# Optimization experiments

Measured on AMD Instinct MI355X. Metric: run time of the kernel, lower is better.

The kernel has to match this reference:

```python
import jax, jax.numpy as jnp
import numpy as np

ALPHA = 0.2
NEG_INF = -9e15


def setup_inputs() -> dict:
    key = jax.random.key(0)
    k1, k2, k3, k4 = jax.random.split(key, 4)
    B, N, C_IN, C_OUT, R, H = 8, 1024, 256, 256, 4, 4
    node_feats = jax.random.normal(k1, (B, N, C_IN), dtype=jnp.float32)
    adj_matrix = jax.random.randint(k2, (B, N, N, R), 0, 2, dtype=jnp.int32)
    # xavier_uniform with gain=1.414 for Linear(c_in, c_out) weights
    lim_w = 1.414 * np.sqrt(6.0 / (C_IN + C_OUT))
    W = jax.random.uniform(k3, (R, C_IN, C_OUT), minval=-lim_w, maxval=lim_w, dtype=jnp.float32)
    c_per = C_OUT // H
    lim_a = 1.414 * np.sqrt(6.0 / (H + 2 * c_per))
    a = jax.random.uniform(k4, (R, H, 2 * c_per), minval=-lim_a, maxval=lim_a, dtype=jnp.float32)
    return {"node_feats": node_feats, "adj_matrix": adj_matrix, "W": W, "a": a}


def reference(node_feats, adj_matrix, W, a):
    B, N, _ = node_feats.shape
    R, H = a.shape[0], a.shape[1]
    C = a.shape[2] // 2  # per-head feature dim
    out = jnp.zeros((B, N, H, C), dtype=node_feats.dtype)
    for r in range(R):
        # per-relation projection: [B,N,H,C]
        f = jnp.einsum('bnc,cd->bnd', node_feats, W[r]).reshape(B, N, H, C)
        a_l, a_r = a[r, :, :C], a[r, :, C:]
        # attention logit decomposes: a . [f_i || f_j] = a_l . f_i + a_r . f_j
        li = jnp.einsum('bnhc,hc->bnh', f, a_l)  # source-node term
        lj = jnp.einsum('bnhc,hc->bnh', f, a_r)  # target-node term
        logits = jax.nn.leaky_relu(li[:, :, None, :] + lj[:, None, :, :], ALPHA)  # [B,N,N,H]
        mask = adj_matrix[..., r] != 0  # [B,N,N]
        logits = jnp.where(mask[..., None], logits, NEG_INF)
        probs = jax.nn.softmax(logits, axis=2)
        out = out + jnp.einsum('bijh,bjhc->bihc', probs, f)
    # concat_heads=True
    return out.reshape(B, N, H * C)
```

## Files before the change

kernel.cpp:

```cpp
#include <hip/hip_runtime.h>
#include <math.h>

#define Bsz 8
#define Nn 1024
#define CIN 256
#define COUT 256
#define NR 4
#define NH 4

typedef unsigned short u16;
typedef __attribute__((ext_vector_type(8))) short bf16x8;
typedef __attribute__((ext_vector_type(4))) float f32x4;
typedef __attribute__((ext_vector_type(2))) float f32x2;

#define OFF_LIP (16u << 20)
#define OFF_LJP ((16u << 20) + (512u << 10))
#define OFF_ADJM (17u << 20)
#define OFF_XBF (21u << 20)
#define OFF_WBFT (25u << 20)
#define OFF_WAL ((25u << 20) + (512u << 10))
#define OFF_WAR ((25u << 20) + (528u << 10))

#define LOG2E 1.4426950408889634f

__device__ __forceinline__ short f2bf(float x) {
  union { float f; unsigned u; } v; v.f = x;
  unsigned r = (v.u + 0x7FFFu + ((v.u >> 16) & 1u)) >> 16;
  return (short)r;
}

__device__ __forceinline__ float fast_exp2(float x) {
#if __has_builtin(__builtin_amdgcn_exp2f)
  return __builtin_amdgcn_exp2f(x);
#else
  return exp2f(x);
#endif
}

__device__ __forceinline__ int sbfe1(unsigned v, int bit) {
#if __has_builtin(__builtin_amdgcn_sbfe)
  return __builtin_amdgcn_sbfe((int)v, bit, 1);
#else
  return ((int)(v << (31 - bit))) >> 31;
#endif
}

__device__ __forceinline__ unsigned perm_hi16(unsigned hi, unsigned lo) {
#if __has_builtin(__builtin_amdgcn_perm)
  return __builtin_amdgcn_perm(hi, lo, 0x07060302u);
#else
  return (lo >> 16) | (hi & 0xFFFF0000u);
#endif
}

__device__ __forceinline__ void gl_lds16(const void* g, void* l) {
  __builtin_amdgcn_global_load_lds(
      (const __attribute__((address_space(1))) unsigned int*)(unsigned long long)g,
      (__attribute__((address_space(3))) unsigned int*)(unsigned int)(unsigned long long)l,
      16, 0, 0);
}

__global__ __launch_bounds__(256, 8)
void gatt_pack(const int4* __restrict__ adj4, unsigned long long* __restrict__ adjm) {
  const int t = threadIdx.x;
  const int wid = blockIdx.x * 4 + (t >> 6);
  const int lane = t & 63;
  const int jw = wid & 15;
  const int i = (wid >> 4) & 1023;
  const int b = wid >> 14;
  const int j = jw * 64 + lane;
  const int4 av = adj4[(size_t)(b * Nn + i) * Nn + j];
  const unsigned long long b0 = __ballot(av.x != 0);
  const unsigned long long b1 = __ballot(av.y != 0);
  const unsigned long long b2 = __ballot(av.z != 0);
  const unsigned long long b3 = __ballot(av.w != 0);
  if (lane < 4) {
    unsigned long long v = (lane == 0) ? b0 : (lane == 1) ? b1 : (lane == 2) ? b2 : b3;
    adjm[((size_t)((b * Nn + i) * NR + lane)) * 16 + jw] = v;
  }
}

__global__ __launch_bounds__(256, 4)
void gatt_prep(const float* __restrict__ W, const float* __restrict__ a,
               u16* __restrict__ WbfT, float* __restrict__ wa_l,
               float* __restrict__ wa_r) {
  const int t = threadIdx.x;
  if (blockIdx.x < 32) {
    const int r = blockIdx.x >> 3, kc = blockIdx.x & 7;
    u16 pk[32];
#pragma unroll 8
    for (int kk = 0; kk < 32; ++kk)
      pk[kk] = (u16)f2bf(W[(size_t)r * 65536 + (size_t)(kc * 32 + kk) * COUT + t]);
    u16* dst = WbfT + (size_t)r * 65536 + (size_t)t * CIN + kc * 32;
#pragma unroll
    for (int q = 0; q < 4; ++q) *(int4*)(dst + q * 8) = *(int4*)(pk + q * 8);
  } else {
    const int cb = blockIdx.x - 32;
    const int r = cb >> 2, h = cb & 3;
    float sl = 0.f, sr = 0.f;
    const float* Wp = W + (size_t)r * 65536 + (size_t)t * COUT + h * 64;
    const float* ap = a + r * 512 + h * 128;
#pragma unroll 8
    for (int c = 0; c < 64; ++c) {
      const float wv = Wp[c];
      sl = fmaf(wv, ap[c], sl);
      sr = fmaf(wv, ap[64 + c], sr);
    }
    wa_l[(size_t)cb * CIN + t] = sl;
    wa_r[(size_t)cb * CIN + t] = sr;
  }
}

__global__ __launch_bounds__(256, 4)
void gatt_logitx(const float* __restrict__ X, const float4* __restrict__ wal4,
                 const float4* __restrict__ war4, float* __restrict__ Lip,
                 float* __restrict__ Ljp, u16* __restrict__ Xbf) {
  __shared__ float Xs[16 * 260];
  const int t = threadIdx.x;
  const int row0 = blockIdx.x * 16;
  {
    const int il = t >> 4, kq = t & 15;
    const float4* xp = (const float4*)(X + (size_t)(row0 + il) * CIN + kq * 16);
    float4 v[4];
    u16 pk[16];
#pragma unroll
    for (int u = 0; u < 4; ++u) {
      v[u] = xp[u];
      pk[u * 4 + 0] = (u16)f2bf(v[u].x);
      pk[u * 4 + 1] = (u16)f2bf(v[u].y);
      pk[u * 4 + 2] = (u16)f2bf(v[u].z);
      pk[u * 4 + 3] = (u16)f2bf(v[u].w);
    }
    float4* dst = (float4*)(Xs + il * 260 + kq * 16);
#pragma unroll
    for (int u = 0; u < 4; ++u) dst[u] = v[u];
    u16* xb = Xbf + (size_t)(row0 + il) * CIN + kq * 16;
    *(int4*)xb = *(int4*)pk;
    *(int4*)(xb + 8) = *(int4*)(pk + 8);
  }
  __syncthreads();
  const int rl = t >> 4, combo = t & 15;
  float li = 0.f, lj = 0.f;
#pragma unroll 8
  for (int k4 = 0; k4 < 64; ++k4) {
    const float4 x4 = *(const float4*)(Xs + rl * 260 + k4 * 4);
    const float4 wl = wal4[combo * 64 + k4];
    const float4 wr = war4[combo * 64 + k4];
    li += x4.x * wl.x + x4.y * wl.y + x4.z * wl.z + x4.w * wl.w;
    lj += x4.x * wr.x + x4.y * wr.y + x4.z * wr.z + x4.w * wr.w;
  }
  const int g = row0 + rl, b = g >> 10, n = g & 1023;
  const size_t idx = ((size_t)(combo * Bsz + b)) * Nn + n;
  Lip[idx] = li * LOG2E;
  Ljp[idx] = lj * LOG2E;
}

__global__ __launch_bounds__(256)
void gatt_fgemm(const u16* __restrict__ Xbf, const u16* __restrict__ WbfT,
                u16* __restrict__ fTf) {
  __shared__ u16 lds_w[8192];
  __shared__ u16 lds_x[2048];
  const int t = threadIdx.x;
  const int r = blockIdx.x & 3, b = (blockIdx.x >> 2) & 7, ntl = blockIdx.x >> 5;
  const int n0 = ntl * 64;
  const int g0 = b * Nn + n0;
  const int lane = t & 63, w = t >> 6;
  const int m = lane & 15, quad = lane >> 4;
  const int cw = w * 64;
  const int xq = quad ^ (m & 3);

  const u16* Wsrc = WbfT + (size_t)r * 65536;
  f32x4 acc[4][4];
#pragma unroll
  for (int ct = 0; ct < 4; ++ct)
#pragma unroll
    for (int nt = 0; nt < 4; ++nt) acc[ct][nt] = (f32x4){0.f, 0.f, 0.f, 0.f};

  for (int kc = 0; kc < 8; ++kc) {
    __syncthreads();
#pragma unroll
    for (int q = 0; q < 4; ++q) {
      const int s = q * 256 + t;
      const int c = s >> 2, ks = (s & 3) ^ (c & 3);
      gl_lds16(Wsrc + (size_t)c * CIN + kc * 32 + ks * 8, lds_w + s * 8);
    }
    {
      const int s = t;
      const int n = s >> 2, ks = (s & 3) ^ (n & 3);
      gl_lds16(Xbf + (size_t)(g0 + n) * CIN + kc * 32 + ks * 8, lds_x + s * 8);
    }
    __syncthreads();

    bf16x8 af[4], bfr[4];
#pragma unroll
    for (int ct = 0; ct < 4; ++ct)
      af[ct] = *(const bf16x8*)(lds_w + (cw + ct * 16 + m) * 32 + xq * 8);
#pragma unroll
    for (int nt = 0; nt < 4; ++nt)
      bfr[nt] = *(const bf16x8*)(lds_x + (nt * 16 + m) * 32 + xq * 8);
#pragma unroll
    for (int ct = 0; ct < 4; ++ct)
#pragma unroll
      for (int nt = 0; nt < 4; ++nt)
        acc[ct][nt] = __builtin_amdgcn_mfma_f32_16x16x32_bf16(af[ct], bfr[nt], acc[ct][nt], 0, 0, 0);
  }

  u16* fragbase = fTf + (size_t)(((r * Bsz + b) * 4 + w) * 128) * 512;
#pragma unroll
  for (int ct = 0; ct < 4; ++ct) {
#pragma unroll
    for (int ntf = 0; ntf < 4; ++ntf) {
      const int j = n0 + ntf * 16 + m;
      const int jb = j >> 5;
      const int qt = ((ntf & 1) << 1) | (m >> 3);
      const int e = m & 7;
      u16* dst = fragbase + (size_t)((jb * 4 + ct) * 512) + (qt * 16 + quad * 4) * 8 + e;
#pragma unroll
      for (int p = 0; p < 4; ++p) dst[p * 8] = (u16)f2bf(acc[ct][ntf][p]);
    }
  }
}

__global__ __launch_bounds__(1024, 4)
void gatt_attn(const unsigned long long* __restrict__ adjm,
               const u16* __restrict__ fTf, const float* __restrict__ Lip,
               const float* __restrict__ Ljp, float* __restrict__ out) {
  __shared__ float smem[16384];

  const int t = threadIdx.x;
  const int b = blockIdx.x & 7;
  const int i0 = (blockIdx.x >> 3) * 32;
  const int w = t >> 6, lane = t & 63;
  const int r = w & 3, h = w >> 2;
  const int m = lane & 15, quad = lane >> 4;
  const int qo = quad * 8;

  {
#pragma unroll
    for (int q = 0; q < 4; ++q) {
      const int s = q * 1024 + t;
      const int combo = s >> 8, off = s & 255;
      ((float4*)smem)[s] =
          ((const float4*)(Ljp + ((size_t)(combo * Bsz + b)) * Nn))[off];
    }
  }
  __syncthreads();

  const float* lipb = Lip + ((size_t)((r * NH + h) * Bsz + b)) * Nn;
  const float li0 = lipb[i0 + m];
  const float li1 = lipb[i0 + 16 + m];
  const unsigned long long* amp0 = adjm + ((size_t)((b * Nn + i0 + m) * NR + r)) * 16;
  const unsigned long long* amp1 = adjm + ((size_t)((b * Nn + i0 + 16 + m) * NR + r)) * 16;
  const bf16x8* fp = (const bf16x8*)fTf + (size_t)(((r * Bsz + b) * 4 + h)) * 8192;
  const float* ljh = smem + (r * NH + h) * Nn;

  bf16x8 ones;
#pragma unroll
  for (int e = 0; e < 8; ++e) ones[e] = (short)0x3F80;

  f32x4 acc[2][4], den[2];
#pragma unroll
  for (int iw = 0; iw < 2; ++iw) {
    den[iw] = (f32x4){0.f, 0.f, 0.f, 0.f};
#pragma unroll
    for (int nt = 0; nt < 4; ++nt) acc[iw][nt] = (f32x4){0.f, 0.f, 0.f, 0.f};
  }

  for (int jq = 0; jq < 16; ++jq) {
    const uint2 mw0 = *(const uint2*)(amp0 + jq);
    const uint2 mw1 = *(const uint2*)(amp1 + jq);
#pragma unroll
    for (int half = 0; half < 2; ++half) {
      const int jb = jq * 2 + half;
      const unsigned w0 = half ? mw0.y : mw0.x;
      const unsigned w1 = half ? mw1.y : mw1.x;
      const f32x2* lj2p = (const f32x2*)(ljh + jb * 32 + qo);
      bf16x8 bfr[4];
#pragma unroll
      for (int nt = 0; nt < 4; ++nt) bfr[nt] = fp[(jb * 4 + nt) * 64 + lane];
#pragma unroll
      for (int iw = 0; iw < 2; ++iw) {
        const float liv = iw ? li1 : li0;
        const unsigned mb = (iw ? w1 : w0) >> qo;
        const f32x2 li2 = {liv, liv};
        unsigned afu[4];
#pragma unroll
        for (int pr = 0; pr < 4; ++pr) {
          const f32x2 s2 = li2 + lj2p[pr];
          const f32x2 s02 = s2 * 0.2f;
          const float t0 = fmaxf(s2.x, s02.x);
          const float t1 = fmaxf(s2.y, s02.y);
          const unsigned e0 =
              __float_as_uint(fast_exp2(t0)) & (unsigned)sbfe1(mb, 2 * pr);
          const unsigned e1 =
              __float_as_uint(fast_exp2(t1)) & (unsigned)sbfe1(mb, 2 * pr + 1);
          afu[pr] = perm_hi16(e1, e0);
        }
        union { unsigned u[4]; bf16x8 v; } af;
        af.u[0] = afu[0]; af.u[1] = afu[1]; af.u[2] = afu[2]; af.u[3] = afu[3];
        den[iw] = __builtin_amdgcn_mfma_f32_16x16x32_bf16(af.v, ones, den[iw], 0, 0, 0);
#pragma unroll
        for (int nt = 0; nt < 4; ++nt)
          acc[iw][nt] = __builtin_amdgcn_mfma_f32_16x16x32_bf16(af.v, bfr[nt], acc[iw][nt], 0, 0, 0);
      }
    }
  }

#define OSTRIDE 260
  __syncthreads();
#pragma unroll
  for (int rr = 0; rr < 4; ++rr) {
    if (r == rr) {
#pragma unroll
      for (int iw = 0; iw < 2; ++iw) {
#pragma unroll
        for (int p = 0; p < 4; ++p) {
          const float inv = __builtin_amdgcn_rcpf(den[iw][p]);
          float* op = smem + (iw * 16 + quad * 4 + p) * OSTRIDE + h * 64 + m;
#pragma unroll
          for (int nt = 0; nt < 4; ++nt) {
            const float v = acc[iw][nt][p] * inv;
            if (rr == 0) op[nt * 16] = v;
            else op[nt * 16] += v;
          }
        }
      }
    }
    __syncthreads();
  }

#pragma unroll
  for (int q = 0; q < 2; ++q) {
    const int idx = q * 1024 + t;
    const int row = idx >> 6, c4 = idx & 63;
    const float4 v = *(const float4*)(smem + row * OSTRIDE + c4 * 4);
    ((float4*)out)[((size_t)(b * Nn + i0 + row)) * 64 + c4] = v;
  }
}

extern "C" void kernel_launch(void* const* d_in, const int* in_sizes, int n_in,
                              void* d_out, int out_size, void* d_ws, size_t ws_size,
                              hipStream_t stream) {
  const float* X = (const float*)d_in[0];
  const int4* adj4 = (const int4*)d_in[1];
  const float* W = (const float*)d_in[2];
  const float* a = (const float*)d_in[3];
  float* out = (float*)d_out;

  char* ws = (char*)d_ws;
  u16* fTf = (u16*)ws;
  float* Lip = (float*)(ws + OFF_LIP);
  float* Ljp = (float*)(ws + OFF_LJP);
  unsigned long long* adjm = (unsigned long long*)(ws + OFF_ADJM);
  u16* Xbf = (u16*)(ws + OFF_XBF);
  u16* WbfT = (u16*)(ws + OFF_WBFT);
  float* wa_l = (float*)(ws + OFF_WAL);
  float* wa_r = (float*)(ws + OFF_WAR);

  gatt_pack<<<dim3(32768), dim3(256), 0, stream>>>(adj4, adjm);
  gatt_prep<<<dim3(48), dim3(256), 0, stream>>>(W, a, WbfT, wa_l, wa_r);
  gatt_logitx<<<dim3(512), dim3(256), 0, stream>>>(X, (const float4*)wa_l,
                                                   (const float4*)wa_r, Lip, Ljp, Xbf);
  gatt_fgemm<<<dim3(512), dim3(256), 0, stream>>>(Xbf, WbfT, fTf);
  gatt_attn<<<dim3(256), dim3(1024), 0, stream>>>(adjm, fTf, Lip, Ljp, out);
}
```

Baseline: 291.3 us.

## Precompute exponentials of logit terms and replace per-pair exp with products

Uses monotonicity of exp2 to rewrite exp2(leaky_relu(li+lj)) as max(exp2(li)exp2(lj), exp2(0.2li)exp2(0.2lj)), with the per-node exponentials precomputed in the logit kernel. The inner attention loop then does multiplies and a max instead of a transcendental per pair. The target-node factors are read from global memory instead of being staged in shared memory, which shrinks LDS use. Products of exponentials can overflow or lose precision for large logits, since there is no max subtraction.

```diff
diff --git a/kernel.cpp b/kernel.cpp
--- a/kernel.cpp
+++ b/kernel.cpp
@@ -13,13 +13,13 @@
 typedef __attribute__((ext_vector_type(4))) float f32x4;
 typedef __attribute__((ext_vector_type(2))) float f32x2;
 
-#define OFF_LIP (16u << 20)
-#define OFF_LJP ((16u << 20) + (512u << 10))
-#define OFF_ADJM (17u << 20)
-#define OFF_XBF (21u << 20)
-#define OFF_WBFT (25u << 20)
-#define OFF_WAL ((25u << 20) + (512u << 10))
-#define OFF_WAR ((25u << 20) + (528u << 10))
+#define OFF_EEI (16u << 20)
+#define OFF_EEJ (17u << 20)
+#define OFF_ADJM (18u << 20)
+#define OFF_XBF (22u << 20)
+#define OFF_WBFT (26u << 20)
+#define OFF_WAL ((26u << 20) + (512u << 10))
+#define OFF_WAR ((26u << 20) + (528u << 10))
 
 #define LOG2E 1.4426950408889634f
 
@@ -113,8 +113,8 @@
 
 __global__ __launch_bounds__(256, 4)
 void gatt_logitx(const float* __restrict__ X, const float4* __restrict__ wal4,
-                 const float4* __restrict__ war4, float* __restrict__ Lip,
-                 float* __restrict__ Ljp, u16* __restrict__ Xbf) {
+                 const float4* __restrict__ war4, float2* __restrict__ EEi,
+                 float2* __restrict__ EEj, u16* __restrict__ Xbf) {
   __shared__ float Xs[16 * 260];
   const int t = threadIdx.x;
   const int row0 = blockIdx.x * 16;
@@ -151,8 +151,9 @@
   }
   const int g = row0 + rl, b = g >> 10, n = g & 1023;
   const size_t idx = ((size_t)(combo * Bsz + b)) * Nn + n;
-  Lip[idx] = li * LOG2E;
-  Ljp[idx] = lj * LOG2E;
+  const float lis = li * LOG2E, ljs = lj * LOG2E;
+  EEi[idx] = make_float2(fast_exp2(lis), fast_exp2(0.2f * lis));
+  EEj[idx] = make_float2(fast_exp2(ljs), fast_exp2(0.2f * ljs));
 }
 
 __global__ __launch_bounds__(256)
@@ -223,9 +224,9 @@
 
 __global__ __launch_bounds__(1024, 4)
 void gatt_attn(const unsigned long long* __restrict__ adjm,
-               const u16* __restrict__ fTf, const float* __restrict__ Lip,
-               const float* __restrict__ Ljp, float* __restrict__ out) {
-  __shared__ float smem[16384];
+               const u16* __restrict__ fTf, const float2* __restrict__ EEi,
+               const float2* __restrict__ EEj, float* __restrict__ out) {
+  __shared__ float smem[32 * 260];
 
   const int t = threadIdx.x;
   const int b = blockIdx.x & 7;
@@ -234,25 +235,18 @@
   const int r = w & 3, h = w >> 2;
   const int m = lane & 15, quad = lane >> 4;
   const int qo = quad * 8;
-
-  {
-#pragma unroll
-    for (int q = 0; q < 4; ++q) {
-      const int s = q * 1024 + t;
-      const int combo = s >> 8, off = s & 255;
-      ((float4*)smem)[s] =
-          ((const float4*)(Ljp + ((size_t)(combo * Bsz + b)) * Nn))[off];
-    }
-  }
-  __syncthreads();
-
-  const float* lipb = Lip + ((size_t)((r * NH + h) * Bsz + b)) * Nn;
-  const float li0 = lipb[i0 + m];
-  const float li1 = lipb[i0 + 16 + m];
+  const int combo = r * NH + h;
+
+  const float2* EEib = EEi + ((size_t)(combo * Bsz + b)) * Nn;
+  const float2 Li0 = EEib[i0 + m];
+  const float2 Li1 = EEib[i0 + 16 + m];
+  const f32x2 EI0 = {Li0.x, Li0.y};
+  const f32x2 EI1 = {Li1.x, Li1.y};
+  const float4* EEj4p = (const float4*)(EEj + ((size_t)(combo * Bsz + b)) * Nn);
+
   const unsigned long long* amp0 = adjm + ((size_t)((b * Nn + i0 + m) * NR + r)) * 16;
   const unsigned long long* amp1 = adjm + ((size_t)((b * Nn + i0 + 16 + m) * NR + r)) * 16;
   const bf16x8* fp = (const bf16x8*)fTf + (size_t)(((r * Bsz + b) * 4 + h)) * 8192;
-  const float* ljh = smem + (r * NH + h) * Nn;
 
   bf16x8 ones;
 #pragma unroll
@@ -272,37 +266,47 @@
 #pragma unroll
     for (int half = 0; half < 2; ++half) {
       const int jb = jq * 2 + half;
-      const unsigned w0 = half ? mw0.y : mw0.x;
-      const unsigned w1 = half ? mw1.y : mw1.x;
-      const f32x2* lj2p = (const f32x2*)(ljh + jb * 32 + qo);
+      const unsigned mb0 = (half ? mw0.y : mw0.x) >> qo;
+      const unsigned mb1 = (half ? mw1.y : mw1.x) >> qo;
       bf16x8 bfr[4];
 #pragma unroll
       for (int nt = 0; nt < 4; ++nt) bfr[nt] = fp[(jb * 4 + nt) * 64 + lane];
-#pragma unroll
-      for (int iw = 0; iw < 2; ++iw) {
-        const float liv = iw ? li1 : li0;
-        const unsigned mb = (iw ? w1 : w0) >> qo;
-        const f32x2 li2 = {liv, liv};
-        unsigned afu[4];
-#pragma unroll
-        for (int pr = 0; pr < 4; ++pr) {
-          const f32x2 s2 = li2 + lj2p[pr];
-          const f32x2 s02 = s2 * 0.2f;
-          const float t0 = fmaxf(s2.x, s02.x);
-          const float t1 = fmaxf(s2.y, s02.y);
+      unsigned afu0[4], afu1[4];
+#pragma unroll
+      for (int pr = 0; pr < 4; ++pr) {
+        const float4 v = EEj4p[jb * 16 + quad * 4 + pr];
+        const f32x2 v01 = {v.x, v.y};
+        const f32x2 v23 = {v.z, v.w};
+        {
+          const f32x2 a0 = v01 * EI0;
+          const f32x2 a1 = v23 * EI0;
           const unsigned e0 =
-              __float_as_uint(fast_exp2(t0)) & (unsigned)sbfe1(mb, 2 * pr);
+              __float_as_uint(fmaxf(a0.x, a0.y)) & (unsigned)sbfe1(mb0, 2 * pr);
           const unsigned e1 =
-              __float_as_uint(fast_exp2(t1)) & (unsigned)sbfe1(mb, 2 * pr + 1);
-          afu[pr] = perm_hi16(e1, e0);
+              __float_as_uint(fmaxf(a1.x, a1.y)) & (unsigned)sbfe1(mb0, 2 * pr + 1);
+          afu0[pr] = perm_hi16(e1, e0);
         }
-        union { unsigned u[4]; bf16x8 v; } af;
-        af.u[0] = afu[0]; af.u[1] = afu[1]; af.u[2] = afu[2]; af.u[3] = afu[3];
-        den[iw] = __builtin_amdgcn_mfma_f32_16x16x32_bf16(af.v, ones, den[iw], 0, 0, 0);
-#pragma unroll
-        for (int nt = 0; nt < 4; ++nt)
-          acc[iw][nt] = __builtin_amdgcn_mfma_f32_16x16x32_bf16(af.v, bfr[nt], acc[iw][nt], 0, 0, 0);
+        {
+          const f32x2 a0 = v01 * EI1;
+          const f32x2 a1 = v23 * EI1;
+          const unsigned e0 =
+              __float_as_uint(fmaxf(a0.x, a0.y)) & (unsigned)sbfe1(mb1, 2 * pr);
+          const unsigned e1 =
+              __float_as_uint(fmaxf(a1.x, a1.y)) & (unsigned)sbfe1(mb1, 2 * pr + 1);
+          afu1[pr] = perm_hi16(e1, e0);
+        }
       }
+      union { unsigned u[4]; bf16x8 v; } af0, af1;
+#pragma unroll
+      for (int pr = 0; pr < 4; ++pr) { af0.u[pr] = afu0[pr]; af1.u[pr] = afu1[pr]; }
+      den[0] = __builtin_amdgcn_mfma_f32_16x16x32_bf16(af0.v, ones, den[0], 0, 0, 0);
+#pragma unroll
+      for (int nt = 0; nt < 4; ++nt)
+        acc[0][nt] = __builtin_amdgcn_mfma_f32_16x16x32_bf16(af0.v, bfr[nt], acc[0][nt], 0, 0, 0);
+      den[1] = __builtin_amdgcn_mfma_f32_16x16x32_bf16(af1.v, ones, den[1], 0, 0, 0);
+#pragma unroll
+      for (int nt = 0; nt < 4; ++nt)
+        acc[1][nt] = __builtin_amdgcn_mfma_f32_16x16x32_bf16(af1.v, bfr[nt], acc[1][nt], 0, 0, 0);
     }
   }
 
@@ -349,8 +353,8 @@
 
   char* ws = (char*)d_ws;
   u16* fTf = (u16*)ws;
-  float* Lip = (float*)(ws + OFF_LIP);
-  float* Ljp = (float*)(ws + OFF_LJP);
+  float2* EEi = (float2*)(ws + OFF_EEI);
+  float2* EEj = (float2*)(ws + OFF_EEJ);
   unsigned long long* adjm = (unsigned long long*)(ws + OFF_ADJM);
   u16* Xbf = (u16*)(ws + OFF_XBF);
   u16* WbfT = (u16*)(ws + OFF_WBFT);
@@ -360,7 +364,7 @@
   gatt_pack<<<dim3(32768), dim3(256), 0, stream>>>(adj4, adjm);
   gatt_prep<<<dim3(48), dim3(256), 0, stream>>>(W, a, WbfT, wa_l, wa_r);
   gatt_logitx<<<dim3(512), dim3(256), 0, stream>>>(X, (const float4*)wa_l,
-                                                   (const float4*)wa_r, Lip, Ljp, Xbf);
+                                                   (const float4*)wa_r, EEi, EEj, Xbf);
   gatt_fgemm<<<dim3(512), dim3(256), 0, stream>>>(Xbf, WbfT, fTf);
-  gatt_attn<<<dim3(256), dim3(1024), 0, stream>>>(adjm, fTf, Lip, Ljp, out);
-}
+  gatt_attn<<<dim3(256), dim3(1024), 0, stream>>>(adjm, fTf, EEi, EEj, out);
+}
```

Result: slower. 304.7 us (+4.6%).
